# Kernel optimization log

Hardware: AMD Instinct MI355X
Metric: run time of the kernel (lower is better)

## Reference

```python
import jax, jax.numpy as jnp
import numpy as np

B, K = 32768, 8            # batch, neighbor count (n_agents)
OBS0, OBS1, OBS2 = 80, 160, 384  # critic_obs[i]*n_agents(*n_agents)
D = 256                    # hidden dim
NH, DH = 3, 256            # n_heads, single_head_dim (768/3)


def setup_inputs() -> dict:
    key = jax.random.key(0)
    ks = jax.random.split(key, 24)

    def w(k, shape):
        return jax.random.normal(k, shape, dtype=jnp.float32) * 0.05

    inp = {
        "state0": jax.random.normal(ks[0], (B, 1, OBS0), dtype=jnp.float32),
        "state1": jax.random.normal(ks[1], (B, 1, OBS1), dtype=jnp.float32),
        "state2": jax.random.normal(ks[2], (B, K, OBS2), dtype=jnp.float32),
        # sum_own_fc / sum_env_fc / sum_sur_fc  (Linear + ReLU)
        "W_own": w(ks[3], (OBS0, D)), "b_own": w(ks[4], (D,)),
        "W_env": w(ks[5], (OBS1, D)), "b_env": w(ks[6], (D,)),
        "W_sur": w(ks[7], (OBS2, D)), "b_sur": w(ks[8], (D,)),
        # sum_q / sum_k / sum_v (no bias)
        "Wq": w(ks[9], (D, D)), "Wk": w(ks[10], (D, D)), "Wv": w(ks[11], (D, D)),
        # com_q / com_k / com_v (no bias), operate on single_head_dim
        "Wcq": w(ks[12], (DH, DH)), "Wck": w(ks[13], (DH, DH)), "Wcv": w(ks[14], (DH, DH)),
        # multi_att_out: 768 -> 128
        "W_out": w(ks[15], (NH * DH, 128)), "b_out": w(ks[16], (128,)),
        # judgement_fc: 128 -> 64 -> 1
        "W_j1": w(ks[17], (128, 64)), "b_j1": w(ks[18], (64,)),
        "W_j2": w(ks[19], (64, 1)), "b_j2": w(ks[20], (1,)),
    }
    return inp


def reference(state0, state1, state2, W_own, b_own, W_env, b_env, W_sur, b_sur,
              Wq, Wk, Wv, Wcq, Wck, Wcv, W_out, b_out, W_j1, b_j1, W_j2, b_j2):
    relu = jax.nn.relu
    sum_own_e = relu(state0 @ W_own + b_own)   # (B,1,D)
    sum_env_e = relu(state1 @ W_env + b_env)   # (B,1,D)
    sum_sur = relu(state2 @ W_sur + b_sur)     # (B,K,D)

    q = sum_own_e @ Wq                          # (B,1,D)
    k = sum_sur @ Wk                            # (B,K,D)
    v = sum_sur @ Wv                            # (B,K,D)

    # mask = state2.mean(axis=2, keepdim=True).bool()  -> True where mean != 0
    mask = jnp.mean(state2, axis=2, keepdims=True) != 0.0      # (B,K,1) bool
    score = jnp.einsum('bkd,bsd->bks', k, q)                   # (B,K,1)
    score = jnp.where(mask, score, -jnp.inf)
    alpha = jax.nn.softmax(score / np.sqrt(D).astype(np.float32), axis=1)
    alpha = jnp.where(mask, alpha, 0.0)
    v_att = jnp.sum(v * alpha, axis=1)                         # (B,D)

    cc = jnp.concatenate([sum_own_e[:, 0], sum_env_e[:, 0], v_att], axis=1)  # (B,768)

    # manual multi-head self attention over seq_len = 1
    raw = cc.reshape(B, 1, NH, DH)            # raw_k == raw_q == raw_v
    comQ = (raw @ Wcq).transpose(0, 2, 1, 3)  # (B,NH,1,DH)  (com_q applied to raw_k, as in source)
    comK = (raw @ Wck).transpose(0, 2, 1, 3)
    comV = (raw @ Wcv).transpose(0, 2, 1, 3)
    product = jnp.einsum('bhqd,bhkd->bhqk', comQ, comK) / np.sqrt(DH).astype(np.float32)
    scores = jax.nn.softmax(product, axis=-1) @ comV           # (B,NH,1,DH)
    concat = scores.transpose(0, 2, 1, 3).reshape(B, 1, NH * DH)

    multi_out = concat @ W_out + b_out                          # (B,1,128)
    hidden = relu(multi_out @ W_j1 + b_j1)                      # (B,1,64)
    q_val = hidden @ W_j2 + b_j2                                # (B,1,1)
    return q_val
```

## Files before the change

### kernel.cpp

```cpp
#include <hip/hip_runtime.h>
#include <hip/hip_bf16.h>
#include <math.h>


typedef unsigned int u32;
typedef __attribute__((ext_vector_type(8))) short bf16x8;
typedef __attribute__((ext_vector_type(4))) float f32x4;

#define KN     8
#define OBS0V  80
#define OBS1V  160
#define OBS2V  384
#define DD     256
#define MB     16

__device__ inline void gl2lds16(const void* g, void* l) {
    __builtin_amdgcn_global_load_lds(
        (const __attribute__((address_space(1))) u32*)g,
        (__attribute__((address_space(3))) u32*)l, 16, 0, 0);
}

__device__ inline ushort f2bf(float x) {
    union { __hip_bfloat16 h; ushort u; } c;
    c.h = __float2bfloat16(x);
    return c.u;
}
__device__ inline float bf2f(ushort u) {
    union { ushort s[2]; float f; } c;
    c.s[0] = 0; c.s[1] = u;
    return c.f;
}
__device__ inline void pack_store8(void* dst, float4 a, float4 b) {
    union { ushort u[8]; uint4 q; } pk;
    pk.u[0]=f2bf(a.x); pk.u[1]=f2bf(a.y); pk.u[2]=f2bf(a.z); pk.u[3]=f2bf(a.w);
    pk.u[4]=f2bf(b.x); pk.u[5]=f2bf(b.y); pk.u[6]=f2bf(b.z); pk.u[7]=f2bf(b.w);
    *(uint4*)dst = pk.q;
}

__global__ void precompute_M(const float* __restrict__ Wk,
                             const float* __restrict__ Wq,
                             float* __restrict__ Mt) {
    __shared__ float wq[DD];
    const int l = blockIdx.x, i = threadIdx.x;
    wq[i] = Wq[l * DD + i];
    __syncthreads();
    const float4* wk4 = (const float4*)(Wk + (size_t)i * DD);
    float acc = 0.f;
#pragma unroll 8
    for (int j = 0; j < DD / 4; ++j) {
        const float4 a = wk4[j];
        const float4 b = *(const float4*)&wq[j * 4];
        acc += a.x * b.x + a.y * b.y + a.z * b.z + a.w * b.w;
    }
    Mt[l * DD + i] = acc;
}

__global__ void precompute_Weff(const float* __restrict__ Wcv,
                                const float* __restrict__ Wout,
                                float* __restrict__ Weff) {
    const int bh = blockIdx.x;
    const int h = bh >> 8, i = bh & 255;
    const int o = threadIdx.x;
    const float* wrow = Wcv + (size_t)i * DD;
    float acc = 0.f;
#pragma unroll 4
    for (int j = 0; j < DD; ++j)
        acc += wrow[j] * Wout[(size_t)(h * DD + j) * 128 + o];
    Weff[(size_t)bh * 128 + o] = acc;
}

__global__ void layout_all(const float* __restrict__ Wown, const float* __restrict__ Wenv,
                           const float* __restrict__ Wsur, const float* __restrict__ Mt2f,
                           const float* __restrict__ Wvf,  const float* __restrict__ Wefff,
                           ushort* __restrict__ pre) {
    const int idx8 = blockIdx.x * blockDim.x + threadIdx.x;
    if (idx8 >= 49152) return;
    const float* src; int Ksrc, N, NT, local;
    if (idx8 < 3072)       { src=Wown;  Ksrc=80;  N=256; NT=16; local=idx8;        }
    else if (idx8 < 8192)  { src=Wenv;  Ksrc=160; N=256; NT=16; local=idx8-3072;   }
    else if (idx8 < 20480) { src=Wsur;  Ksrc=384; N=256; NT=16; local=idx8-8192;   }
    else if (idx8 < 28672) { src=Mt2f;  Ksrc=256; N=256; NT=16; local=idx8-20480;  }
    else if (idx8 < 36864) { src=Wvf;   Ksrc=256; N=256; NT=16; local=idx8-28672;  }
    else                   { src=Wefff; Ksrc=768; N=128; NT=8;  local=idx8-36864;  }
    const int lane = local & 63;
    const int nt   = (local >> 6) & (NT - 1);
    const int kc   = local / (64 * NT);
    const int n    = nt * 16 + (lane & 15);
    const int k0   = kc * 32 + (lane >> 4) * 8;
    union { ushort u[8]; uint4 q; } pk;
#pragma unroll
    for (int j = 0; j < 8; ++j) {
        const int k = k0 + j;
        pk.u[j] = (k < Ksrc) ? f2bf(src[(size_t)k * N + n]) : (ushort)0;
    }
    *(uint4*)(pre + (size_t)idx8 * 8) = pk.q;
}

template<int NCH, int NTT, int NTW>
__device__ inline void gemm16(const char* sA, int strideA, const ushort* wpre,
                              char* swb, f32x4* acc, int w, int lane) {
    const int lm = lane & 15, lq = lane >> 4;
#pragma unroll
    for (int n = 0; n < NTW; ++n) acc[n] = (f32x4){0.f, 0.f, 0.f, 0.f};
    const int chunkB = NTT * 1024;
    const int perwave = chunkB / 4;
    for (int kc = 0; kc < NCH; ++kc) {
        __syncthreads();
        const char* src = (const char*)wpre + (size_t)kc * chunkB;
        for (int i = 0; i < perwave; i += 1024)
            gl2lds16(src + w * perwave + i + lane * 16, swb + w * perwave + i);
        __syncthreads();
        const bf16x8 af = *(const bf16x8*)(sA + lm * strideA + kc * 64 + lq * 16);
#pragma unroll
        for (int n = 0; n < NTW; ++n) {
            const bf16x8 bfr = *(const bf16x8*)(swb + ((size_t)(w * NTW + n) * 64 + lane) * 16);
            acc[n] = __builtin_amdgcn_mfma_f32_16x16x32_bf16(af, bfr, acc[n], 0, 0, 0);
        }
    }
}

__global__ __launch_bounds__(256, 2) void critic_mfma(
    const float* __restrict__ state0, const float* __restrict__ state1,
    const float* __restrict__ state2,
    const float* __restrict__ b_own, const float* __restrict__ b_env,
    const float* __restrict__ b_sur, const float* __restrict__ b_out,
    const float* __restrict__ W_j1, const float* __restrict__ b_j1,
    const float* __restrict__ W_j2, const float* __restrict__ b_j2,
    const ushort* __restrict__ pre_own, const ushort* __restrict__ pre_env,
    const ushort* __restrict__ pre_sur, const ushort* __restrict__ pre_mt2,
    const ushort* __restrict__ pre_wv,  const ushort* __restrict__ pre_weff,
    float* __restrict__ out) {

    __shared__ __align__(16) ushort s_cc[MB * 776];
    __shared__ __align__(16) ushort s_att[MB * 264];
    __shared__ __align__(16) char   s_w[16384];
    __shared__ __align__(16) char   s_a[10240];
    __shared__ float s_spart[2 * 128];
    __shared__ float s_alpha[128];
    __shared__ float s_mask[128];

    const int t = threadIdx.x;
    const int lane = t & 63;
    const int w = t >> 6;
    const int lm = lane & 15, lq = lane >> 4;
    const int bbase = blockIdx.x * MB;

    {
        uint4 z; z.x = z.y = z.z = z.w = 0u;
        for (int i = t; i < 640; i += 256) ((uint4*)s_a)[i] = z;
    }
    __syncthreads();

    if (t < 160) {
        const int row = t / 10, s = t % 10;
        const float* gp = state0 + (size_t)(bbase + row) * OBS0V + s * 8;
        pack_store8(s_a + row * 240 + s * 16, *(const float4*)gp, *(const float4*)(gp + 4));
    }
    __syncthreads();

    {
        f32x4 acc[4];
        gemm16<3, 16, 4>((const char*)s_a, 240, pre_own, s_w, acc, w, lane);
#pragma unroll
        for (int n = 0; n < 4; ++n) {
            const int gc = (w * 4 + n) * 16 + lm;
            const float bv = b_own[gc];
#pragma unroll
            for (int r = 0; r < 4; ++r)
                s_cc[(size_t)(lq * 4 + r) * 776 + gc] = f2bf(fmaxf(acc[n][r] + bv, 0.f));
        }
    }
    __syncthreads();

    {
        const int row = t / 20, s = t % 20;
        const float* gp = state1 + (size_t)(bbase + row) * OBS1V + s * 8;
        pack_store8(s_a + row * 336 + s * 16, *(const float4*)gp, *(const float4*)(gp + 4));
        if (t < 64) {
            const int slot = t + 256, row2 = slot / 20, s2 = slot % 20;
            const float* gp2 = state1 + (size_t)(bbase + row2) * OBS1V + s2 * 8;
            pack_store8(s_a + row2 * 336 + s2 * 16, *(const float4*)gp2, *(const float4*)(gp2 + 4));
        }
    }
    __syncthreads();

    {
        f32x4 acc[4];
        gemm16<5, 16, 4>((const char*)s_a, 336, pre_env, s_w, acc, w, lane);
#pragma unroll
        for (int n = 0; n < 4; ++n) {
            const int gc = (w * 4 + n) * 16 + lm;
            const float bv = b_env[gc];
#pragma unroll
            for (int r = 0; r < 4; ++r)
                s_cc[(size_t)(lq * 4 + r) * 776 + 256 + gc] = f2bf(fmaxf(acc[n][r] + bv, 0.f));
        }
    }
    __syncthreads();

    {
        f32x4 acc[4];
        gemm16<8, 16, 4>((const char*)s_cc, 1552, pre_mt2, s_w, acc, w, lane);
#pragma unroll
        for (int n = 0; n < 4; ++n) {
            const int gc = (w * 4 + n) * 16 + lm;
#pragma unroll
            for (int r = 0; r < 4; ++r)
                s_cc[(size_t)(lq * 4 + r) * 776 + 512 + gc] = f2bf(acc[n][r]);
        }
    }

    f32x4 sacc[4][8];
#pragma unroll
    for (int a = 0; a < 4; ++a)
#pragma unroll
        for (int b2 = 0; b2 < 8; ++b2) sacc[a][b2] = (f32x4){0.f, 0.f, 0.f, 0.f};
    float ms0 = 0.f, ms1 = 0.f;
    const int wm = w & 1, wn = w >> 1;
    const float* s2b = state2 + (size_t)bbase * KN * OBS2V;
    const int row0 = t >> 2, q0 = t & 3;

    for (int kc = 0; kc < 12; ++kc) {
        __syncthreads();
        const char* wsrc = (const char*)pre_sur + (size_t)kc * 16384;
        for (int i = 0; i < 4096; i += 1024)
            gl2lds16(wsrc + w * 4096 + i + lane * 16, s_w + w * 4096 + i);
        {
            const float* gp = s2b + (size_t)row0 * OBS2V + kc * 32 + q0 * 8;
            const float4 a0 = *(const float4*)gp;
            const float4 a1 = *(const float4*)(gp + 4);
            ms0 += a0.x + a0.y + a0.z + a0.w + a1.x + a1.y + a1.z + a1.w;
            pack_store8(s_a + row0 * 80 + q0 * 16, a0, a1);
            const float* gp1 = gp + (size_t)64 * OBS2V;
            const float4 c0 = *(const float4*)gp1;
            const float4 c1 = *(const float4*)(gp1 + 4);
            ms1 += c0.x + c0.y + c0.z + c0.w + c1.x + c1.y + c1.z + c1.w;
            pack_store8(s_a + (64 + row0) * 80 + q0 * 16, c0, c1);
        }
        __syncthreads();
        bf16x8 bfr[8];
#pragma unroll
        for (int n = 0; n < 8; ++n)
            bfr[n] = *(const bf16x8*)(s_w + ((size_t)(wn * 8 + n) * 64 + lane) * 16);
#pragma unroll
        for (int mt = 0; mt < 4; ++mt) {
            const int rowa = (wm * 4 + mt) * 16 + lm;
            const bf16x8 af = *(const bf16x8*)(s_a + rowa * 80 + lq * 16);
#pragma unroll
            for (int n = 0; n < 8; ++n)
                sacc[mt][n] = __builtin_amdgcn_mfma_f32_16x16x32_bf16(af, bfr[n], sacc[mt][n], 0, 0, 0);
        }
    }
    {
        float p = ms0;
        p += __shfl_xor(p, 1); p += __shfl_xor(p, 2);
        if (q0 == 0) s_mask[row0] = p;
        float p2 = ms1;
        p2 += __shfl_xor(p2, 1); p2 += __shfl_xor(p2, 2);
        if (q0 == 0) s_mask[64 + row0] = p2;
    }
    {
        float bs[8];
#pragma unroll
        for (int n = 0; n < 8; ++n) bs[n] = b_sur[wn * 128 + n * 16 + lm];
#pragma unroll
        for (int mt = 0; mt < 4; ++mt)
#pragma unroll
            for (int n = 0; n < 8; ++n)
#pragma unroll
                for (int r = 0; r < 4; ++r)
                    sacc[mt][n][r] = fmaxf(sacc[mt][n][r] + bs[n], 0.f);
    }
#pragma unroll
    for (int mt = 0; mt < 4; ++mt) {
        const int tm = wm * 4 + mt;
        const int bb = 2 * tm + (lq >> 1);
        float u8[8];
#pragma unroll
        for (int n = 0; n < 8; ++n)
            u8[n] = bf2f(s_cc[(size_t)bb * 776 + 512 + wn * 128 + n * 16 + lm]);
#pragma unroll
        for (int r = 0; r < 4; ++r) {
            float p = 0.f;
#pragma unroll
            for (int n = 0; n < 8; ++n) p += sacc[mt][n][r] * u8[n];
            p += __shfl_xor(p, 1); p += __shfl_xor(p, 2);
            p += __shfl_xor(p, 4); p += __shfl_xor(p, 8);
            if (lm == 0) s_spart[wn * 128 + tm * 16 + lq * 4 + r] = p;
        }
    }
    __syncthreads();
    if (t < MB) {
        float sc[8]; float mx = -INFINITY;
#pragma unroll
        for (int k = 0; k < 8; ++k) {
            const int row = t * 8 + k;
            const float s = s_spart[row] + s_spart[128 + row];
            sc[k] = (s_mask[row] != 0.f) ? s * 0.0625f : -INFINITY;
            mx = fmaxf(mx, sc[k]);
        }
        float e[8]; float dn = 0.f;
#pragma unroll
        for (int k = 0; k < 8; ++k) {
            e[k] = (sc[k] == -INFINITY) ? 0.f : __expf(sc[k] - mx);
            dn += e[k];
        }
        const float inv = (dn > 0.f) ? 1.f / dn : 0.f;
#pragma unroll
        for (int k = 0; k < 8; ++k) s_alpha[t * 8 + k] = e[k] * inv;
    }
    __syncthreads();
#pragma unroll
    for (int mt = 0; mt < 4; ++mt) {
        const int tm = wm * 4 + mt;
        float al[4];
#pragma unroll
        for (int r = 0; r < 4; ++r) al[r] = s_alpha[tm * 16 + lq * 4 + r];
#pragma unroll
        for (int n = 0; n < 8; ++n) {
            float p = sacc[mt][n][0] * al[0] + sacc[mt][n][1] * al[1]
                    + sacc[mt][n][2] * al[2] + sacc[mt][n][3] * al[3];
            p += __shfl_xor(p, 16);
            const int col = wn * 128 + n * 16 + lm;
            if (lq == 0)      s_att[(size_t)(2 * tm) * 264 + col] = f2bf(p);
            else if (lq == 2) s_att[(size_t)(2 * tm + 1) * 264 + col] = f2bf(p);
        }
    }
    __syncthreads();

    {
        f32x4 acc[4];
        gemm16<8, 16, 4>((const char*)s_att, 528, pre_wv, s_w, acc, w, lane);
#pragma unroll
        for (int n = 0; n < 4; ++n) {
            const int gc = (w * 4 + n) * 16 + lm;
#pragma unroll
            for (int r = 0; r < 4; ++r)
                s_cc[(size_t)(lq * 4 + r) * 776 + 512 + gc] = f2bf(acc[n][r]);
        }
    }
    __syncthreads();

    float* s_multi = (float*)s_a;
    {
        f32x4 acc[2];
        gemm16<24, 8, 2>((const char*)s_cc, 1552, pre_weff, s_w, acc, w, lane);
#pragma unroll
        for (int n = 0; n < 2; ++n) {
            const int gc = (w * 2 + n) * 16 + lm;
            const float bv = b_out[gc];
#pragma unroll
            for (int r = 0; r < 4; ++r)
                s_multi[(lq * 4 + r) * 128 + gc] = acc[n][r] + bv;
        }
    }
    __syncthreads();

    float hid[4];
#pragma unroll
    for (int p = 0; p < 4; ++p) {
        const int idx = t + 256 * p;
        const int b2 = idx >> 6, h = idx & 63;
        float a2 = b_j1[h];
#pragma unroll 4
        for (int o = 0; o < 128; ++o) a2 += s_multi[b2 * 128 + o] * W_j1[o * 64 + h];
        hid[p] = fmaxf(a2, 0.f);
    }
    float* s_hid = (float*)s_att;
    __syncthreads();
#pragma unroll
    for (int p = 0; p < 4; ++p) {
        const int idx = t + 256 * p;
        s_hid[(idx >> 6) * 64 + (idx & 63)] = hid[p];
    }
    __syncthreads();
    if (t < MB) {
        float a2 = b_j2[0];
#pragma unroll 4
        for (int h = 0; h < 64; ++h) a2 += s_hid[t * 64 + h] * W_j2[h];
        out[bbase + t] = a2;
    }
}

extern "C" void kernel_launch(void* const* d_in, const int* in_sizes, int n_in,
                              void* d_out, int out_size, void* d_ws, size_t ws_size,
                              hipStream_t stream) {
    (void)n_in; (void)out_size; (void)ws_size;
    const float* state0 = (const float*)d_in[0];
    const float* state1 = (const float*)d_in[1];
    const float* state2 = (const float*)d_in[2];
    const float* W_own  = (const float*)d_in[3];
    const float* b_own  = (const float*)d_in[4];
    const float* W_env  = (const float*)d_in[5];
    const float* b_env  = (const float*)d_in[6];
    const float* W_sur  = (const float*)d_in[7];
    const float* b_sur  = (const float*)d_in[8];
    const float* Wq     = (const float*)d_in[9];
    const float* Wk     = (const float*)d_in[10];
    const float* Wv     = (const float*)d_in[11];
    const float* Wcv    = (const float*)d_in[14];
    const float* W_out  = (const float*)d_in[15];
    const float* b_out  = (const float*)d_in[16];
    const float* W_j1   = (const float*)d_in[17];
    const float* b_j1   = (const float*)d_in[18];
    const float* W_j2   = (const float*)d_in[19];
    const float* b_j2   = (const float*)d_in[20];
    float* out = (float*)d_out;

    float* Mt2f  = (float*)d_ws;
    float* Wefff = Mt2f + 65536;
    ushort* pre  = (ushort*)((char*)d_ws + 655360);
    ushort* pre_own  = pre;
    ushort* pre_env  = pre + 24576;
    ushort* pre_sur  = pre + 65536;
    ushort* pre_mt2  = pre + 163840;
    ushort* pre_wv   = pre + 229376;
    ushort* pre_weff = pre + 294912;

    const int B = in_sizes[0] / OBS0V;

    precompute_M<<<256, 256, 0, stream>>>(Wk, Wq, Mt2f);
    precompute_Weff<<<768, 128, 0, stream>>>(Wcv, W_out, Wefff);
    layout_all<<<192, 256, 0, stream>>>(W_own, W_env, W_sur, Mt2f, Wv, Wefff, pre);
    critic_mfma<<<B / MB, 256, 0, stream>>>(state0, state1, state2,
        b_own, b_env, b_sur, b_out, W_j1, b_j1, W_j2, b_j2,
        pre_own, pre_env, pre_sur, pre_mt2, pre_wv, pre_weff, out);
}
```

Before: 795.4 us.

## Read MFMA weights from global directly and double-buffer state2 tiles in LDS

Drops the LDS staging of pre-swizzled weights and the two barriers per K-chunk. Each wave now loads its B fragments straight from global (L2-cached) memory. The state2 GEMM loop gains a register prefetch of the next chunk and double-buffered LDS tiles, cutting to one barrier per iteration, and the first state2 loads are issued before the Mt2 GEMM. The judgement MLP tail is restructured so each thread reuses loaded weights across four rows, and the final dot product is split across lanes. In exchange, every block re-reads weights from cache, which adds global traffic and latency, and the extra LDS buffer may affect occupancy.

```diff
diff --git a/kernel.cpp b/kernel.cpp
--- a/kernel.cpp
+++ b/kernel.cpp
@@ -3,7 +3,6 @@
 #include <math.h>
 
 
-typedef unsigned int u32;
 typedef __attribute__((ext_vector_type(8))) short bf16x8;
 typedef __attribute__((ext_vector_type(4))) float f32x4;
 
@@ -13,12 +12,6 @@
 #define OBS2V  384
 #define DD     256
 #define MB     16
-
-__device__ inline void gl2lds16(const void* g, void* l) {
-    __builtin_amdgcn_global_load_lds(
-        (const __attribute__((address_space(1))) u32*)g,
-        (__attribute__((address_space(3))) u32*)l, 16, 0, 0);
-}
 
 __device__ inline ushort f2bf(float x) {
     union { __hip_bfloat16 h; ushort u; } c;
@@ -96,24 +89,19 @@
     *(uint4*)(pre + (size_t)idx8 * 8) = pk.q;
 }
 
-template<int NCH, int NTT, int NTW>
-__device__ inline void gemm16(const char* sA, int strideA, const ushort* wpre,
-                              char* swb, f32x4* acc, int w, int lane) {
+template<int NCH, int NT, int NTW>
+__device__ inline void gemm_reg(const char* sA, int strideA, const ushort* wpre,
+                                f32x4* acc, int w, int lane) {
     const int lm = lane & 15, lq = lane >> 4;
 #pragma unroll
     for (int n = 0; n < NTW; ++n) acc[n] = (f32x4){0.f, 0.f, 0.f, 0.f};
-    const int chunkB = NTT * 1024;
-    const int perwave = chunkB / 4;
+#pragma unroll 4
     for (int kc = 0; kc < NCH; ++kc) {
-        __syncthreads();
-        const char* src = (const char*)wpre + (size_t)kc * chunkB;
-        for (int i = 0; i < perwave; i += 1024)
-            gl2lds16(src + w * perwave + i + lane * 16, swb + w * perwave + i);
-        __syncthreads();
         const bf16x8 af = *(const bf16x8*)(sA + lm * strideA + kc * 64 + lq * 16);
 #pragma unroll
         for (int n = 0; n < NTW; ++n) {
-            const bf16x8 bfr = *(const bf16x8*)(swb + ((size_t)(w * NTW + n) * 64 + lane) * 16);
+            const bf16x8 bfr = *(const bf16x8*)(wpre +
+                ((size_t)(kc * NT + w * NTW + n) * 64 + lane) * 8);
             acc[n] = __builtin_amdgcn_mfma_f32_16x16x32_bf16(af, bfr, acc[n], 0, 0, 0);
         }
     }
@@ -133,8 +121,7 @@
 
     __shared__ __align__(16) ushort s_cc[MB * 776];
     __shared__ __align__(16) ushort s_att[MB * 264];
-    __shared__ __align__(16) char   s_w[16384];
-    __shared__ __align__(16) char   s_a[10240];
+    __shared__ __align__(16) char   s_a[2 * 10240];
     __shared__ float s_spart[2 * 128];
     __shared__ float s_alpha[128];
     __shared__ float s_mask[128];
@@ -145,22 +132,21 @@
     const int lm = lane & 15, lq = lane >> 4;
     const int bbase = blockIdx.x * MB;
 
-    {
-        uint4 z; z.x = z.y = z.z = z.w = 0u;
-        for (int i = t; i < 640; i += 256) ((uint4*)s_a)[i] = z;
-    }
-    __syncthreads();
-
-    if (t < 160) {
-        const int row = t / 10, s = t % 10;
-        const float* gp = state0 + (size_t)(bbase + row) * OBS0V + s * 8;
-        pack_store8(s_a + row * 240 + s * 16, *(const float4*)gp, *(const float4*)(gp + 4));
+    if (t < 240) {
+        const int row = t / 15, s = t % 15;
+        if (s < 10) {
+            const float* gp = state0 + (size_t)(bbase + row) * OBS0V + s * 8;
+            pack_store8(s_a + row * 240 + s * 16, *(const float4*)gp, *(const float4*)(gp + 4));
+        } else {
+            uint4 z; z.x = z.y = z.z = z.w = 0u;
+            *(uint4*)(s_a + row * 240 + s * 16) = z;
+        }
     }
     __syncthreads();
 
     {
         f32x4 acc[4];
-        gemm16<3, 16, 4>((const char*)s_a, 240, pre_own, s_w, acc, w, lane);
+        gemm_reg<3, 16, 4>(s_a, 240, pre_own, acc, w, lane);
 #pragma unroll
         for (int n = 0; n < 4; ++n) {
             const int gc = (w * 4 + n) * 16 + lm;
@@ -186,7 +172,7 @@
 
     {
         f32x4 acc[4];
-        gemm16<5, 16, 4>((const char*)s_a, 336, pre_env, s_w, acc, w, lane);
+        gemm_reg<5, 16, 4>(s_a, 336, pre_env, acc, w, lane);
 #pragma unroll
         for (int n = 0; n < 4; ++n) {
             const int gc = (w * 4 + n) * 16 + lm;
@@ -196,60 +182,72 @@
                 s_cc[(size_t)(lq * 4 + r) * 776 + 256 + gc] = f2bf(fmaxf(acc[n][r] + bv, 0.f));
         }
     }
-    __syncthreads();
-
-    {
-        f32x4 acc[4];
-        gemm16<8, 16, 4>((const char*)s_cc, 1552, pre_mt2, s_w, acc, w, lane);
-#pragma unroll
-        for (int n = 0; n < 4; ++n) {
-            const int gc = (w * 4 + n) * 16 + lm;
-#pragma unroll
-            for (int r = 0; r < 4; ++r)
-                s_cc[(size_t)(lq * 4 + r) * 776 + 512 + gc] = f2bf(acc[n][r]);
-        }
-    }
-
-    f32x4 sacc[4][8];
-#pragma unroll
-    for (int a = 0; a < 4; ++a)
-#pragma unroll
-        for (int b2 = 0; b2 < 8; ++b2) sacc[a][b2] = (f32x4){0.f, 0.f, 0.f, 0.f};
-    float ms0 = 0.f, ms1 = 0.f;
+
     const int wm = w & 1, wn = w >> 1;
     const float* s2b = state2 + (size_t)bbase * KN * OBS2V;
     const int row0 = t >> 2, q0 = t & 3;
+    const float* gbase  = s2b + (size_t)row0 * OBS2V + q0 * 8;
+    const float* gbase2 = gbase + (size_t)64 * OBS2V;
+    float4 p_a0 = *(const float4*)gbase;
+    float4 p_a1 = *(const float4*)(gbase + 4);
+    float4 p_c0 = *(const float4*)gbase2;
+    float4 p_c1 = *(const float4*)(gbase2 + 4);
+
+    {
+        f32x4 acc[4];
+        gemm_reg<8, 16, 4>((const char*)s_cc, 1552, pre_mt2, acc, w, lane);
+#pragma unroll
+        for (int n = 0; n < 4; ++n) {
+            const int gc = (w * 4 + n) * 16 + lm;
+#pragma unroll
+            for (int r = 0; r < 4; ++r)
+                s_cc[(size_t)(lq * 4 + r) * 776 + 512 + gc] = f2bf(acc[n][r]);
+        }
+    }
+    __syncthreads();
+
+    float ms0 = 0.f, ms1 = 0.f;
+    ms0 += p_a0.x + p_a0.y + p_a0.z + p_a0.w + p_a1.x + p_a1.y + p_a1.z + p_a1.w;
+    pack_store8(s_a + row0 * 80 + q0 * 16, p_a0, p_a1);
+    ms1 += p_c0.x + p_c0.y + p_c0.z + p_c0.w + p_c1.x + p_c1.y + p_c1.z + p_c1.w;
+    pack_store8(s_a + (64 + row0) * 80 + q0 * 16, p_c0, p_c1);
+    __syncthreads();
+
+    f32x4 sacc[4][8];
+#pragma unroll
+    for (int a = 0; a < 4; ++a)
+#pragma unroll
+        for (int b2 = 0; b2 < 8; ++b2) sacc[a][b2] = (f32x4){0.f, 0.f, 0.f, 0.f};
 
     for (int kc = 0; kc < 12; ++kc) {
-        __syncthreads();
-        const char* wsrc = (const char*)pre_sur + (size_t)kc * 16384;
-        for (int i = 0; i < 4096; i += 1024)
-            gl2lds16(wsrc + w * 4096 + i + lane * 16, s_w + w * 4096 + i);
-        {
-            const float* gp = s2b + (size_t)row0 * OBS2V + kc * 32 + q0 * 8;
-            const float4 a0 = *(const float4*)gp;
-            const float4 a1 = *(const float4*)(gp + 4);
-            ms0 += a0.x + a0.y + a0.z + a0.w + a1.x + a1.y + a1.z + a1.w;
-            pack_store8(s_a + row0 * 80 + q0 * 16, a0, a1);
-            const float* gp1 = gp + (size_t)64 * OBS2V;
-            const float4 c0 = *(const float4*)gp1;
-            const float4 c1 = *(const float4*)(gp1 + 4);
-            ms1 += c0.x + c0.y + c0.z + c0.w + c1.x + c1.y + c1.z + c1.w;
-            pack_store8(s_a + (64 + row0) * 80 + q0 * 16, c0, c1);
-        }
-        __syncthreads();
+        const char* bufc = s_a + (kc & 1) * 10240;
+        char* bufn = s_a + ((kc + 1) & 1) * 10240;
+        float4 na0, na1, nc0, nc1;
+        if (kc < 11) {
+            const float* gp  = gbase  + (kc + 1) * 32;
+            const float* gp2 = gbase2 + (kc + 1) * 32;
+            na0 = *(const float4*)gp;  na1 = *(const float4*)(gp + 4);
+            nc0 = *(const float4*)gp2; nc1 = *(const float4*)(gp2 + 4);
+        }
         bf16x8 bfr[8];
 #pragma unroll
         for (int n = 0; n < 8; ++n)
-            bfr[n] = *(const bf16x8*)(s_w + ((size_t)(wn * 8 + n) * 64 + lane) * 16);
+            bfr[n] = *(const bf16x8*)(pre_sur +
+                ((size_t)(kc * 16 + wn * 8 + n) * 64 + lane) * 8);
 #pragma unroll
         for (int mt = 0; mt < 4; ++mt) {
-            const int rowa = (wm * 4 + mt) * 16 + lm;
-            const bf16x8 af = *(const bf16x8*)(s_a + rowa * 80 + lq * 16);
+            const bf16x8 af = *(const bf16x8*)(bufc + ((wm * 4 + mt) * 16 + lm) * 80 + lq * 16);
 #pragma unroll
             for (int n = 0; n < 8; ++n)
                 sacc[mt][n] = __builtin_amdgcn_mfma_f32_16x16x32_bf16(af, bfr[n], sacc[mt][n], 0, 0, 0);
         }
+        if (kc < 11) {
+            ms0 += na0.x + na0.y + na0.z + na0.w + na1.x + na1.y + na1.z + na1.w;
+            pack_store8(bufn + row0 * 80 + q0 * 16, na0, na1);
+            ms1 += nc0.x + nc0.y + nc0.z + nc0.w + nc1.x + nc1.y + nc1.z + nc1.w;
+            pack_store8(bufn + (64 + row0) * 80 + q0 * 16, nc0, nc1);
+        }
+        __syncthreads();
     }
     {
         float p = ms0;
@@ -330,7 +328,7 @@
 
     {
         f32x4 acc[4];
-        gemm16<8, 16, 4>((const char*)s_att, 528, pre_wv, s_w, acc, w, lane);
+        gemm_reg<8, 16, 4>((const char*)s_att, 528, pre_wv, acc, w, lane);
 #pragma unroll
         for (int n = 0; n < 4; ++n) {
             const int gc = (w * 4 + n) * 16 + lm;
@@ -344,7 +342,7 @@
     float* s_multi = (float*)s_a;
     {
         f32x4 acc[2];
-        gemm16<24, 8, 2>((const char*)s_cc, 1552, pre_weff, s_w, acc, w, lane);
+        gemm_reg<24, 8, 2>((const char*)s_cc, 1552, pre_weff, acc, w, lane);
 #pragma unroll
         for (int n = 0; n < 2; ++n) {
             const int gc = (w * 2 + n) * 16 + lm;
@@ -356,29 +354,40 @@
     }
     __syncthreads();
 
-    float hid[4];
-#pragma unroll
-    for (int p = 0; p < 4; ++p) {
-        const int idx = t + 256 * p;
-        const int b2 = idx >> 6, h = idx & 63;
-        float a2 = b_j1[h];
+    float* s_hid = (float*)s_att;
+    {
+        const int h = t & 63, b0r = t >> 6;
+        const float bj = b_j1[h];
+        float acc0 = bj, acc1 = bj, acc2 = bj, acc3 = bj;
 #pragma unroll 4
-        for (int o = 0; o < 128; ++o) a2 += s_multi[b2 * 128 + o] * W_j1[o * 64 + h];
-        hid[p] = fmaxf(a2, 0.f);
-    }
-    float* s_hid = (float*)s_att;
-    __syncthreads();
-#pragma unroll
-    for (int p = 0; p < 4; ++p) {
-        const int idx = t + 256 * p;
-        s_hid[(idx >> 6) * 64 + (idx & 63)] = hid[p];
-    }
-    __syncthreads();
-    if (t < MB) {
-        float a2 = b_j2[0];
-#pragma unroll 4
-        for (int h = 0; h < 64; ++h) a2 += s_hid[t * 64 + h] * W_j2[h];
-        out[bbase + t] = a2;
+        for (int o4 = 0; o4 < 32; ++o4) {
+            const float w0 = W_j1[(o4 * 4 + 0) * 64 + h];
+            const float w1 = W_j1[(o4 * 4 + 1) * 64 + h];
+            const float w2 = W_j1[(o4 * 4 + 2) * 64 + h];
+            const float w3 = W_j1[(o4 * 4 + 3) * 64 + h];
+            const float4 m0 = *(const float4*)&s_multi[(b0r     ) * 128 + o4 * 4];
+            const float4 m1 = *(const float4*)&s_multi[(b0r +  4) * 128 + o4 * 4];
+            const float4 m2 = *(const float4*)&s_multi[(b0r +  8) * 128 + o4 * 4];
+            const float4 m3 = *(const float4*)&s_multi[(b0r + 12) * 128 + o4 * 4];
+            acc0 += m0.x * w0 + m0.y * w1 + m0.z * w2 + m0.w * w3;
+            acc1 += m1.x * w0 + m1.y * w1 + m1.z * w2 + m1.w * w3;
+            acc2 += m2.x * w0 + m2.y * w1 + m2.z * w2 + m2.w * w3;
+            acc3 += m3.x * w0 + m3.y * w1 + m3.z * w2 + m3.w * w3;
+        }
+        s_hid[(b0r     ) * 64 + h] = fmaxf(acc0, 0.f);
+        s_hid[(b0r +  4) * 64 + h] = fmaxf(acc1, 0.f);
+        s_hid[(b0r +  8) * 64 + h] = fmaxf(acc2, 0.f);
+        s_hid[(b0r + 12) * 64 + h] = fmaxf(acc3, 0.f);
+    }
+    __syncthreads();
+    if (t < 64) {
+        const int b2 = t >> 2, pp = t & 3;
+        float a2 = 0.f;
+#pragma unroll
+        for (int h = 0; h < 16; ++h)
+            a2 += s_hid[b2 * 64 + pp * 16 + h] * W_j2[pp * 16 + h];
+        a2 += __shfl_xor(a2, 1); a2 += __shfl_xor(a2, 2);
+        if (pp == 0) out[bbase + b2] = a2 + b_j2[0];
     }
 }
 
```

Result: faster. 746.8 us (-6.1%).
